# Kernel tuning notes

Measured on AMD Instinct MI355X. Metric: run time of the kernel, lower is better.

## Reference

```python
import jax, jax.numpy as jnp
import numpy as np

ITERATIONS = 20


def setup_inputs() -> dict:
    key = jax.random.key(0)
    x = jax.random.normal(key, (64, 8, 256, 256), dtype=jnp.float32)
    return {"x": x}


def reference(x):
    # Sinkhorn operator in log space: 20 alternating row/col log-softmax,
    # then exponentiate to obtain a (soft) doubly-stochastic matrix.
    def body(i, x):
        x = jax.nn.log_softmax(x, axis=-2)  # normalize columns
        x = jax.nn.log_softmax(x, axis=-1)  # normalize rows
        return x

    x = jax.lax.fori_loop(0, ITERATIONS, body, x)
    return jnp.exp(x)
```

## Files before the change

### kernel.cpp

```cpp
#include <hip/hip_runtime.h>

#define MAT_N 256
#define TPB   1024
#define ITERS 20

template<int CTRL>
__device__ __forceinline__ float dpp_add(float x) {
    int s = __builtin_amdgcn_update_dpp(0, __builtin_bit_cast(int, x), CTRL, 0xF, 0xF, true);
    return x + __builtin_bit_cast(float, s);
}

__device__ __forceinline__ float allreduce32(float x) {
    x = dpp_add<0x121>(x);
    x = dpp_add<0x122>(x);
    x = dpp_add<0x124>(x);
    x = dpp_add<0x128>(x);
    return x + __shfl_xor(x, 16, 64);
}

__device__ __forceinline__ float pairsum32(float x) {
    return x + __shfl_xor(x, 32, 64);
}

__global__ __launch_bounds__(TPB)
__attribute__((amdgpu_waves_per_eu(4, 4)))
void sinkhorn_kernel(const float* __restrict__ x, float* __restrict__ out)
{
    const int t    = threadIdx.x;
    const int tC   = t & 31;
    const int row0 = (t >> 5) << 3;
    const int col0 = tC << 3;
    const int w    = t >> 6;
    const int rot  = (tC >> 2) & 7;
    const int kb   = (t & 32) >> 3;

    const float* __restrict__ xm = x   + (size_t)blockIdx.x * (MAT_N * MAT_N);
    float* __restrict__       om = out + (size_t)blockIdx.x * (MAT_N * MAT_N);

    __shared__ float part[16][MAT_N];
    __shared__ float gvec[MAT_N];

    float E[8][8];
#pragma unroll
    for (int l = 0; l < 8; ++l) {
        const float* rp = xm + (row0 + l) * MAT_N + col0;
        float4 a = *(const float4*)(rp);
        float4 b = *(const float4*)(rp + 4);
        E[l][0] = __expf(a.x); E[l][1] = __expf(a.y);
        E[l][2] = __expf(a.z); E[l][3] = __expf(a.w);
        E[l][4] = __expf(b.x); E[l][5] = __expf(b.y);
        E[l][6] = __expf(b.z); E[l][7] = __expf(b.w);
    }

    float f[8], g[8];
#pragma unroll
    for (int l = 0; l < 8; ++l) f[l] = 1.0f;

    for (int it = 0; it < ITERS; ++it) {
        float p[8];
#pragma unroll
        for (int k = 0; k < 8; ++k) p[k] = E[0][k] * f[0];
#pragma unroll
        for (int l = 1; l < 8; ++l)
#pragma unroll
            for (int k = 0; k < 8; ++k) p[k] += E[l][k] * f[l];
#pragma unroll
        for (int k = 0; k < 8; ++k) p[k] = pairsum32(p[k]);
#pragma unroll
        for (int k = 0; k < 4; ++k) {
            const int kk = kb + k;
            part[w][col0 + ((kk + rot) & 7)] = p[kk];
        }
        __syncthreads();
        if (t < MAT_N) {
            const int pos = (t & ~7) | (((t & 7) + (t >> 5)) & 7);
            float s = 0.0f;
#pragma unroll
            for (int r = 0; r < 16; ++r) s += part[r][pos];
            gvec[t] = __builtin_amdgcn_rcpf(s);
        }
        __syncthreads();

        {
            float4 g0 = *(const float4*)&gvec[col0];
            float4 g1 = *(const float4*)&gvec[col0 + 4];
            g[0] = g0.x; g[1] = g0.y; g[2] = g0.z; g[3] = g0.w;
            g[4] = g1.x; g[5] = g1.y; g[6] = g1.z; g[7] = g1.w;
        }

        float q[8];
#pragma unroll
        for (int l = 0; l < 8; ++l) {
            float s = E[l][0] * g[0];
#pragma unroll
            for (int k = 1; k < 8; ++k) s += E[l][k] * g[k];
            q[l] = s;
        }
#pragma unroll
        for (int l = 0; l < 8; ++l) {
            q[l] = allreduce32(q[l]);
            f[l] = __builtin_amdgcn_rcpf(q[l]);
        }
    }

#pragma unroll
    for (int l = 0; l < 8; ++l) {
        float fr = f[l];
        float* rp = om + (row0 + l) * MAT_N + col0;
        *(float4*)(rp)     = make_float4(E[l][0] * fr * g[0], E[l][1] * fr * g[1],
                                         E[l][2] * fr * g[2], E[l][3] * fr * g[3]);
        *(float4*)(rp + 4) = make_float4(E[l][4] * fr * g[4], E[l][5] * fr * g[5],
                                         E[l][6] * fr * g[6], E[l][7] * fr * g[7]);
    }
}

extern "C" void kernel_launch(void* const* d_in, const int* in_sizes, int n_in,
                              void* d_out, int out_size, void* d_ws, size_t ws_size,
                              hipStream_t stream) {
    const float* x = (const float*)d_in[0];
    float* out = (float*)d_out;
    const int nmat = in_sizes[0] / (MAT_N * MAT_N);
    sinkhorn_kernel<<<nmat, TPB, 0, stream>>>(x, out);
}
```

Baseline: 311.4 us.

## Store exp matrix in packed fp16 and halve threads per block

```diff
diff --git a/kernel.cpp b/kernel.cpp
--- a/kernel.cpp
+++ b/kernel.cpp
@@ -1,116 +1,175 @@
 #include <hip/hip_runtime.h>
 
 #define MAT_N 256
-#define TPB   1024
+#define TPB   512
 #define ITERS 20
+
+typedef _Float16 half2v __attribute__((ext_vector_type(2)));
 
 template<int CTRL>
 __device__ __forceinline__ float dpp_add(float x) {
     int s = __builtin_amdgcn_update_dpp(0, __builtin_bit_cast(int, x), CTRL, 0xF, 0xF, true);
     return x + __builtin_bit_cast(float, s);
 }
-
-__device__ __forceinline__ float allreduce32(float x) {
+__device__ __forceinline__ float allreduce16(float x) {
     x = dpp_add<0x121>(x);
     x = dpp_add<0x122>(x);
     x = dpp_add<0x124>(x);
     x = dpp_add<0x128>(x);
-    return x + __shfl_xor(x, 16, 64);
+    return x;
 }
 
-__device__ __forceinline__ float pairsum32(float x) {
-    return x + __shfl_xor(x, 32, 64);
+__device__ __forceinline__ half2v pkrtz(float lo, float hi) {
+    return __builtin_bit_cast(half2v, __builtin_amdgcn_cvt_pkrtz(lo, hi));
 }
+
+#if __has_builtin(__builtin_amdgcn_fdot2)
+__device__ __forceinline__ float dot2(half2v a, half2v b, float c) {
+    return __builtin_amdgcn_fdot2(a, b, c, false);
+}
+#else
+__device__ __forceinline__ float dot2(half2v a, half2v b, float c) {
+    return c + (float)a.x * (float)b.x + (float)a.y * (float)b.y;
+}
+#endif
 
 __global__ __launch_bounds__(TPB)
 __attribute__((amdgpu_waves_per_eu(4, 4)))
 void sinkhorn_kernel(const float* __restrict__ x, float* __restrict__ out)
 {
     const int t    = threadIdx.x;
-    const int tC   = t & 31;
-    const int row0 = (t >> 5) << 3;
-    const int col0 = tC << 3;
-    const int w    = t >> 6;
-    const int rot  = (tC >> 2) & 7;
-    const int kb   = (t & 32) >> 3;
+    const int tC   = t & 15;
+    const int tR   = t >> 4;
+    const int row0 = tR << 3;
+    const int col0 = tC << 4;
 
-    const float* __restrict__ xm = x   + (size_t)blockIdx.x * (MAT_N * MAT_N);
-    float* __restrict__       om = out + (size_t)blockIdx.x * (MAT_N * MAT_N);
+    const size_t moff = (size_t)blockIdx.x * (MAT_N * MAT_N);
+    const float* __restrict__ xm = x + moff;
+    float* __restrict__       om = out + moff;
 
-    __shared__ float part[16][MAT_N];
-    __shared__ float gvec[MAT_N];
+    __shared__ half2v part[32][132];
+    __shared__ float  gvec[MAT_N];
 
-    float E[8][8];
+    half2v E[8][8];
 #pragma unroll
     for (int l = 0; l < 8; ++l) {
         const float* rp = xm + (row0 + l) * MAT_N + col0;
-        float4 a = *(const float4*)(rp);
-        float4 b = *(const float4*)(rp + 4);
-        E[l][0] = __expf(a.x); E[l][1] = __expf(a.y);
-        E[l][2] = __expf(a.z); E[l][3] = __expf(a.w);
-        E[l][4] = __expf(b.x); E[l][5] = __expf(b.y);
-        E[l][6] = __expf(b.z); E[l][7] = __expf(b.w);
+        float4 a = ((const float4*)rp)[0];
+        float4 b = ((const float4*)rp)[1];
+        float4 c = ((const float4*)rp)[2];
+        float4 d = ((const float4*)rp)[3];
+        E[l][0] = (half2v){(_Float16)__expf(a.x), (_Float16)__expf(a.y)};
+        E[l][1] = (half2v){(_Float16)__expf(a.z), (_Float16)__expf(a.w)};
+        E[l][2] = (half2v){(_Float16)__expf(b.x), (_Float16)__expf(b.y)};
+        E[l][3] = (half2v){(_Float16)__expf(b.z), (_Float16)__expf(b.w)};
+        E[l][4] = (half2v){(_Float16)__expf(c.x), (_Float16)__expf(c.y)};
+        E[l][5] = (half2v){(_Float16)__expf(c.z), (_Float16)__expf(c.w)};
+        E[l][6] = (half2v){(_Float16)__expf(d.x), (_Float16)__expf(d.y)};
+        E[l][7] = (half2v){(_Float16)__expf(d.z), (_Float16)__expf(d.w)};
     }
 
-    float f[8], g[8];
+    float  f[8];
+    half2v f2[8];
 #pragma unroll
-    for (int l = 0; l < 8; ++l) f[l] = 1.0f;
+    for (int l = 0; l < 8; ++l) {
+        f[l]  = 1.0f;
+        f2[l] = (half2v){(_Float16)1.0f, (_Float16)1.0f};
+    }
+    half2v g2[8];
 
     for (int it = 0; it < ITERS; ++it) {
-        float p[8];
+        half2v p2[8];
 #pragma unroll
-        for (int k = 0; k < 8; ++k) p[k] = E[0][k] * f[0];
+        for (int k = 0; k < 8; ++k) p2[k] = E[0][k] * f2[0];
 #pragma unroll
         for (int l = 1; l < 8; ++l)
 #pragma unroll
-            for (int k = 0; k < 8; ++k) p[k] += E[l][k] * f[l];
-#pragma unroll
-        for (int k = 0; k < 8; ++k) p[k] = pairsum32(p[k]);
-#pragma unroll
-        for (int k = 0; k < 4; ++k) {
-            const int kk = kb + k;
-            part[w][col0 + ((kk + rot) & 7)] = p[kk];
+            for (int k = 0; k < 8; ++k) p2[k] += E[l][k] * f2[l];
+
+        {
+            half2v* wp = &part[tR][tC << 3];
+            float4 w0 = make_float4(__builtin_bit_cast(float, p2[0]),
+                                    __builtin_bit_cast(float, p2[1]),
+                                    __builtin_bit_cast(float, p2[2]),
+                                    __builtin_bit_cast(float, p2[3]));
+            float4 w1 = make_float4(__builtin_bit_cast(float, p2[4]),
+                                    __builtin_bit_cast(float, p2[5]),
+                                    __builtin_bit_cast(float, p2[6]),
+                                    __builtin_bit_cast(float, p2[7]));
+            ((float4*)wp)[0] = w0;
+            ((float4*)wp)[1] = w1;
         }
         __syncthreads();
-        if (t < MAT_N) {
-            const int pos = (t & ~7) | (((t & 7) + (t >> 5)) & 7);
-            float s = 0.0f;
+
+        if (t < 128) {
+            float slo = 0.0f, shi = 0.0f;
 #pragma unroll
-            for (int r = 0; r < 16; ++r) s += part[r][pos];
-            gvec[t] = __builtin_amdgcn_rcpf(s);
+            for (int r = 0; r < 32; ++r) {
+                half2v v = part[r][t];
+                slo += (float)v.x;
+                shi += (float)v.y;
+            }
+            float2 gw;
+            gw.x = __builtin_amdgcn_rcpf(slo);
+            gw.y = __builtin_amdgcn_rcpf(shi);
+            *(float2*)&gvec[t << 1] = gw;
         }
         __syncthreads();
 
         {
-            float4 g0 = *(const float4*)&gvec[col0];
-            float4 g1 = *(const float4*)&gvec[col0 + 4];
-            g[0] = g0.x; g[1] = g0.y; g[2] = g0.z; g[3] = g0.w;
-            g[4] = g1.x; g[5] = g1.y; g[6] = g1.z; g[7] = g1.w;
+            const float* gp = &gvec[col0];
+            float4 a = ((const float4*)gp)[0];
+            float4 b = ((const float4*)gp)[1];
+            float4 c = ((const float4*)gp)[2];
+            float4 d = ((const float4*)gp)[3];
+            g2[0] = pkrtz(a.x, a.y);
+            g2[1] = pkrtz(a.z, a.w);
+            g2[2] = pkrtz(b.x, b.y);
+            g2[3] = pkrtz(b.z, b.w);
+            g2[4] = pkrtz(c.x, c.y);
+            g2[5] = pkrtz(c.z, c.w);
+            g2[6] = pkrtz(d.x, d.y);
+            g2[7] = pkrtz(d.z, d.w);
         }
 
-        float q[8];
 #pragma unroll
         for (int l = 0; l < 8; ++l) {
-            float s = E[l][0] * g[0];
+            float s = dot2(E[l][0], g2[0], 0.0f);
 #pragma unroll
-            for (int k = 1; k < 8; ++k) s += E[l][k] * g[k];
-            q[l] = s;
-        }
-#pragma unroll
-        for (int l = 0; l < 8; ++l) {
-            q[l] = allreduce32(q[l]);
-            f[l] = __builtin_amdgcn_rcpf(q[l]);
+            for (int k = 1; k < 8; ++k) s = dot2(E[l][k], g2[k], s);
+            s = allreduce16(s);
+            f[l] = __builtin_amdgcn_rcpf(s);
+            _Float16 h = (_Float16)f[l];
+            f2[l] = (half2v){h, h};
         }
     }
 
+    float g[16];
+    {
+        const float* gp = &gvec[col0];
+        float4 a = ((const float4*)gp)[0];
+        float4 b = ((const float4*)gp)[1];
+        float4 c = ((const float4*)gp)[2];
+        float4 d = ((const float4*)gp)[3];
+        g[0]=a.x;  g[1]=a.y;  g[2]=a.z;  g[3]=a.w;
+        g[4]=b.x;  g[5]=b.y;  g[6]=b.z;  g[7]=b.w;
+        g[8]=c.x;  g[9]=c.y;  g[10]=c.z; g[11]=c.w;
+        g[12]=d.x; g[13]=d.y; g[14]=d.z; g[15]=d.w;
+    }
 #pragma unroll
     for (int l = 0; l < 8; ++l) {
         float fr = f[l];
         float* rp = om + (row0 + l) * MAT_N + col0;
-        *(float4*)(rp)     = make_float4(E[l][0] * fr * g[0], E[l][1] * fr * g[1],
-                                         E[l][2] * fr * g[2], E[l][3] * fr * g[3]);
-        *(float4*)(rp + 4) = make_float4(E[l][4] * fr * g[4], E[l][5] * fr * g[5],
-                                         E[l][6] * fr * g[6], E[l][7] * fr * g[7]);
+        float o[16];
+#pragma unroll
+        for (int k = 0; k < 8; ++k) {
+            o[2*k]   = (float)E[l][k].x * fr * g[2*k];
+            o[2*k+1] = (float)E[l][k].y * fr * g[2*k+1];
+        }
+        ((float4*)rp)[0] = make_float4(o[0],  o[1],  o[2],  o[3]);
+        ((float4*)rp)[1] = make_float4(o[4],  o[5],  o[6],  o[7]);
+        ((float4*)rp)[2] = make_float4(o[8],  o[9],  o[10], o[11]);
+        ((float4*)rp)[3] = make_float4(o[12], o[13], o[14], o[15]);
     }
 }
 
```

Measured after the change: 270.8 us. 13.0% less time.
